# Optimization experiments

Hardware: AMD Instinct MI355X
Metric: run time of the kernel (lower is better)

The kernel has to match this reference:

```python
import jax, jax.numpy as jnp
import numpy as np

B, T, D = 2, 2048, 2048
N, K, H = 16, 4, 128  # query heads, kv heads, head dim
G = N // K            # GQA groups
MIN_TS, MAX_TS = 1.0, 10000.0


def rope(x, positions):
    # x: [B, S, heads, H], positions: [B, S] int
    half = H // 2
    fraction = 2.0 * jnp.arange(half, dtype=jnp.float32) / H
    timescale = MIN_TS * (MAX_TS / MIN_TS) ** fraction            # [half]
    sinusoid = positions.astype(jnp.float32)[:, :, None, None] / timescale  # [B,S,1,half]
    sin, cos = jnp.sin(sinusoid), jnp.cos(sinusoid)
    x1, x2 = x[..., :half], x[..., half:]
    return jnp.concatenate([x1 * cos - x2 * sin, x2 * cos + x1 * sin], axis=-1)


def setup_inputs() -> dict:
    key = jax.random.key(0)
    ks = jax.random.split(key, 6)
    pos = jnp.tile(jnp.arange(T, dtype=jnp.int32)[None, :], (B, 1))
    return {
        "Xq": jax.random.normal(ks[0], (B, T, D), jnp.float32),
        "Xkv": jax.random.normal(ks[1], (B, T, D), jnp.float32),
        "q_positions": pos,
        "kv_positions": pos,
        "Wq": jax.random.normal(ks[2], (D, N, H), jnp.float32) * 0.02,
        "Wk": jax.random.normal(ks[3], (D, K, H), jnp.float32) * 0.02,
        "Wv": jax.random.normal(ks[4], (D, K, H), jnp.float32) * 0.02,
        "Wo": jax.random.normal(ks[5], (N, H, D), jnp.float32) * 0.02,
    }


def reference(Xq, Xkv, q_positions, kv_positions, Wq, Wk, Wv, Wo):
    # QKV projections (tensordot over embed dim), fp32
    q = jnp.einsum("btd,dnh->btnh", Xq, Wq)          # [B,T,N,H]
    k = jnp.einsum("bsd,dkh->bskh", Xkv, Wk)         # [B,S,K,H]
    v = jnp.einsum("bsd,dkh->bskh", Xkv, Wv)
    # inline RoPE on q and k
    q = rope(q, q_positions)
    k = rope(k, kv_positions)
    # GQA: group query heads over kv heads -> [B,K,G,T,H]
    qg = q.transpose(0, 2, 1, 3).reshape(B, K, G, T, H)
    kt = k.transpose(0, 2, 1, 3)                      # [B,K,S,H]
    vt = v.transpose(0, 2, 1, 3)
    scale = 1.0 / jnp.sqrt(jnp.float32(H))
    scores = jnp.einsum("bkgth,bksh->bkgts", qg, kt) * scale
    # causal mask (self-attn, no explicit mask, T>1)
    causal = jnp.tril(jnp.ones((T, T), dtype=bool))
    scores = jnp.where(causal[None, None, None], scores, jnp.finfo(scores.dtype).min)
    probs = jax.nn.softmax(scores, axis=-1)
    attn = jnp.einsum("bkgts,bksh->bkgth", probs, vt)  # [B,K,G,T,H]
    attn = attn.reshape(B, N, T, H).transpose(0, 2, 1, 3)  # [B,T,N,H]
    out = jnp.einsum("btnh,nhd->btd", attn, Wo)
    return out
```

## Files before the change

### kernel.cpp

```cpp
#include <hip/hip_runtime.h>
#include <hip/hip_bf16.h>
#include <cstdint>
#include <cstddef>

#define Bdim 2
#define Tdim 2048
#define Ddim 2048
#define NHq  16
#define NKV  4
#define HD   128
#define SCALE 0.08838834764831845f
#define QPRESCALE (0.08838834764831845f * 1.4426950408889634f)
#define NEG_INF (-3.0e38f)
#define DEFER_THR 11.5f
#define ROPE_L2 0.20762051f
#define INV_2PI 0.15915494f

typedef unsigned short u16;
typedef unsigned int   u32;
typedef __bf16 bf16x8 __attribute__((ext_vector_type(8)));
typedef float  f32x4  __attribute__((ext_vector_type(4)));

__device__ __forceinline__ u16 f2bf(float f) {
    unsigned int u = __float_as_uint(f);
    u += 0x7FFFu + ((u >> 16) & 1u);
    return (u16)(u >> 16);
}
__device__ __forceinline__ u16 f2bfn(float f) {
    __bf16 h = (__bf16)f;
    return __builtin_bit_cast(u16, h);
}
__device__ __forceinline__ float bf2f(u16 s) {
    return __uint_as_float(((unsigned int)s) << 16);
}

__device__ __forceinline__ void hw_sincos_rev(float rev, float* s, float* c) {
    rev -= floorf(rev);
    *s = __builtin_amdgcn_sinf(rev);
    *c = __builtin_amdgcn_cosf(rev);
}

#if __has_builtin(__builtin_amdgcn_permlane16_swap) && __has_builtin(__builtin_amdgcn_permlane32_swap)
#define HAVE_PERMLANE_SWAP 1
#endif

__device__ __forceinline__ float quad_reduce_max(float v) {
#ifdef HAVE_PERMLANE_SWAP
    auto r = __builtin_amdgcn_permlane16_swap(__float_as_uint(v), __float_as_uint(v), false, false);
    float m = fmaxf(__uint_as_float(r[0]), __uint_as_float(r[1]));
    auto r2 = __builtin_amdgcn_permlane32_swap(__float_as_uint(m), __float_as_uint(m), false, false);
    return fmaxf(__uint_as_float(r2[0]), __uint_as_float(r2[1]));
#else
    v = fmaxf(v, __shfl_xor(v, 16));
    return fmaxf(v, __shfl_xor(v, 32));
#endif
}
__device__ __forceinline__ float quad_reduce_sum(float v) {
#ifdef HAVE_PERMLANE_SWAP
    auto r = __builtin_amdgcn_permlane16_swap(__float_as_uint(v), __float_as_uint(v), false, false);
    float s = __uint_as_float(r[0]) + __uint_as_float(r[1]);
    auto r2 = __builtin_amdgcn_permlane32_swap(__float_as_uint(s), __float_as_uint(s), false, false);
    return __uint_as_float(r2[0]) + __uint_as_float(r2[1]);
#else
    v += __shfl_xor(v, 16);
    return v + __shfl_xor(v, 32);
#endif
}

__device__ __forceinline__ float tree_max16(const float (&s)[16]) {
    float a0 = fmaxf(s[0], s[1]),  a1 = fmaxf(s[2], s[3]);
    float a2 = fmaxf(s[4], s[5]),  a3 = fmaxf(s[6], s[7]);
    float a4 = fmaxf(s[8], s[9]),  a5 = fmaxf(s[10], s[11]);
    float a6 = fmaxf(s[12], s[13]), a7 = fmaxf(s[14], s[15]);
    float b0 = fmaxf(a0, a1), b1 = fmaxf(a2, a3);
    float b2 = fmaxf(a4, a5), b3 = fmaxf(a6, a7);
    return fmaxf(fmaxf(b0, b1), fmaxf(b2, b3));
}
__device__ __forceinline__ float tree_sum16(const float (&s)[16]) {
    float a0 = s[0] + s[1],  a1 = s[2] + s[3];
    float a2 = s[4] + s[5],  a3 = s[6] + s[7];
    float a4 = s[8] + s[9],  a5 = s[10] + s[11];
    float a6 = s[12] + s[13], a7 = s[14] + s[15];
    float b0 = a0 + a1, b1 = a2 + a3, b2 = a4 + a5, b3 = a6 + a7;
    return (b0 + b1) + (b2 + b3);
}

typedef __attribute__((address_space(1))) const u32 gbl_u32;
typedef __attribute__((address_space(3))) u32 lds_u32;
__device__ __forceinline__ void gload16(const void* g, void* l) {
    __builtin_amdgcn_global_load_lds((gbl_u32*)(uintptr_t)g, (lds_u32*)(uintptr_t)l, 16, 0, 0);
}

#define VM8 asm volatile("s_waitcnt vmcnt(8)" ::: "memory")
#define VM6 asm volatile("s_waitcnt vmcnt(6)" ::: "memory")
#define VM4 asm volatile("s_waitcnt vmcnt(4)" ::: "memory")
#define VM3 asm volatile("s_waitcnt vmcnt(3)" ::: "memory")
#define VM0 asm volatile("s_waitcnt vmcnt(0)" ::: "memory")
#define VMNONE ((void)0)
#define BARRIER do { asm volatile("" ::: "memory"); __builtin_amdgcn_s_barrier(); asm volatile("" ::: "memory"); } while (0)

__global__ __launch_bounds__(256) void prep_all(const float* __restrict__ Xq,
                                                const float* __restrict__ Xkv,
                                                const float* __restrict__ Wq,
                                                const float* __restrict__ Wk,
                                                const float* __restrict__ Wv,
                                                const float* __restrict__ Wo,
                                                u16* __restrict__ xq_bf,
                                                u16* __restrict__ xkv_bf,
                                                u16* __restrict__ wq_t,
                                                u16* __restrict__ wk_t,
                                                u16* __restrict__ wv_t,
                                                u16* __restrict__ wo_t)
{
    __shared__ u16 t[64][72];
    const int tid = threadIdx.x;
    int bid = blockIdx.x;

    if (bid < 8192) {
        const size_t NE = (size_t)4096 * 2048 / 8;
        size_t idx = (size_t)bid * 256 + tid;
        const float* src; u16* dst; size_t off;
        if (idx < NE) { src = Xq;  dst = xq_bf;  off = idx * 8; }
        else          { src = Xkv; dst = xkv_bf; off = (idx - NE) * 8; }
        float4 a = *(const float4*)&src[off];
        float4 b = *(const float4*)&src[off + 4];
        ushort4 r0, r1;
        r0.x = f2bf(a.x); r0.y = f2bf(a.y); r0.z = f2bf(a.z); r0.w = f2bf(a.w);
        r1.x = f2bf(b.x); r1.y = f2bf(b.y); r1.z = f2bf(b.z); r1.w = f2bf(b.w);
        *(ushort4*)&dst[off] = r0;
        *(ushort4*)&dst[off + 4] = r1;
        return;
    }
    bid -= 8192;
    const float* src; u16* dst; int C, gx;
    const int R = 2048;
    if (bid < 1024)      { src = Wq; dst = wq_t; C = 2048; gx = 32; }
    else if (bid < 1280) { src = Wk; dst = wk_t; C = 512;  gx = 8;  bid -= 1024; }
    else if (bid < 1536) { src = Wv; dst = wv_t; C = 512;  gx = 8;  bid -= 1280; }
    else                 { src = Wo; dst = wo_t; C = 2048; gx = 32; bid -= 1536; }

    const int r0 = (bid / gx) * 64, c0 = (bid % gx) * 64;
    const int tr = tid >> 4, tc4 = (tid & 15) * 4;
#pragma unroll
    for (int p = 0; p < 4; p++) {
        int r = p * 16 + tr;
        float4 v = *(const float4*)&src[(size_t)(r0 + r) * C + c0 + tc4];
        t[tc4 + 0][r] = f2bf(v.x);
        t[tc4 + 1][r] = f2bf(v.y);
        t[tc4 + 2][r] = f2bf(v.z);
        t[tc4 + 3][r] = f2bf(v.w);
    }
    __syncthreads();
#pragma unroll
    for (int p = 0; p < 4; p++) {
        int cc = p * 16 + tr;
        ushort4 w = *(const ushort4*)&t[cc][tc4];
        *(ushort4*)&dst[(size_t)(c0 + cc) * R + r0 + tc4] = w;
    }
}

__global__ __launch_bounds__(256) void rope_k(u16* __restrict__ k,
                                              const int* __restrict__ kvpos)
{
    int idx = blockIdx.x * 256 + threadIdx.x;
    int rn = idx >> 4;
    int h4 = (idx & 15) * 4;
    int pos = kvpos[rn >> 2];
    u16* base = k + (size_t)rn * HD;
    ushort4 a = *(const ushort4*)&base[h4];
    ushort4 bvec = *(const ushort4*)&base[h4 + 64];
    u16 av[4] = {a.x, a.y, a.z, a.w};
    u16 bv[4] = {bvec.x, bvec.y, bvec.z, bvec.w};
#pragma unroll
    for (int j = 0; j < 4; j++) {
        float rscale = __builtin_amdgcn_exp2f((float)(h4 + j) * -ROPE_L2) * INV_2PI;
        float s, c;
        hw_sincos_rev((float)pos * rscale, &s, &c);
        float x1 = bf2f(av[j]), x2 = bf2f(bv[j]);
        av[j] = f2bf(x1 * c - x2 * s);
        bv[j] = f2bf(x2 * c + x1 * s);
    }
    ushort4 ra, rb;
    ra.x = av[0]; ra.y = av[1]; ra.z = av[2]; ra.w = av[3];
    rb.x = bv[0]; rb.y = bv[1]; rb.z = bv[2]; rb.w = bv[3];
    *(ushort4*)&base[h4] = ra;
    *(ushort4*)&base[h4 + 64] = rb;
}

#define GPH(c, ks, mh, STAGE, VMW) do {                                        \
    bf16x8 Af[4];                                                              \
    _Pragma("unroll")                                                          \
    for (int mf = 0; mf < 4; mf++)                                             \
        Af[mf] = *(const bf16x8*)&Ab[c][ks][(arow + (mh) * 64 + mf * 16) * 32 + cxs]; \
    if ((mh) == 0) {                                                           \
        _Pragma("unroll")                                                      \
        for (int nf = 0; nf < 4; nf++)                                         \
            Bf[nf] = *(const bf16x8*)&Bb[c][ks][(brow + nf * 16) * 32 + cxs];  \
    }                                                                          \
    STAGE;                                                                     \
    BARRIER;                                                                   \
    asm volatile("s_waitcnt lgkmcnt(0)" ::: "memory");                         \
    __builtin_amdgcn_s_setprio(1);                                             \
    _Pragma("unroll")                                                          \
    for (int mf = 0; mf < 4; mf++)                                             \
        _Pragma("unroll")                                                      \
        for (int nf = 0; nf < 4; nf++)                                         \
            acc[(mh) * 4 + mf][nf] = __builtin_amdgcn_mfma_f32_16x16x32_bf16(  \
                Af[mf], Bf[nf], acc[(mh) * 4 + mf][nf], 0, 0, 0);              \
    __builtin_amdgcn_s_setprio(0);                                             \
    VMW;                                                                       \
    BARRIER;                                                                   \
} while (0)

__device__ __forceinline__ void gemm8_mainloop(const u16* __restrict__ A,
                                               const u16* __restrict__ Bt,
                                               int m0, int n0,
                                               u16 (&Ab)[2][2][256 * 32],
                                               u16 (&Bb)[2][2][256 * 32],
                                               f32x4 (&acc)[8][4])
{
    const int tid = threadIdx.x;
    const int wv = tid >> 6, lane = tid & 63;
    const int l15 = lane & 15, quad = lane >> 4;
    const int wr = wv >> 2, wc = wv & 3;

#pragma unroll
    for (int mf = 0; mf < 8; mf++)
#pragma unroll
        for (int nf = 0; nf < 4; nf++) acc[mf][nf] = (f32x4){0.f, 0.f, 0.f, 0.f};

    auto stageA = [&](int kt, int kh, int c) {
#pragma unroll
        for (int j = 0; j < 2; j++) {
            int q = j * 512 + tid;
            int r = q >> 2;
            int c4 = (q & 3) ^ (r & 3);
            gload16(A + (size_t)(m0 + r) * 2048 + kt * 64 + kh * 32 + c4 * 8,
                    &Ab[c][kh][q * 8]);
        }
    };
    auto stageB = [&](int kt, int kh, int c) {
#pragma unroll
        for (int j = 0; j < 2; j++) {
            int q = j * 512 + tid;
            int r = q >> 2;
            int c4 = (q & 3) ^ (r & 3);
            gload16(Bt + (size_t)(n0 + r) * 2048 + kt * 64 + kh * 32 + c4 * 8,
                    &Bb[c][kh][q * 8]);
        }
    };

    const int arow = wr * 128 + l15;
    const int brow = wc * 64 + l15;
    const int cxs  = (quad ^ (l15 & 3)) * 8;

    stageA(0, 0, 0); stageB(0, 0, 0);
    stageA(0, 1, 0); stageB(0, 1, 0);
    stageA(1, 0, 1); stageB(1, 0, 1);
    VM8;
    BARRIER;

    bf16x8 Bf[4];
    for (int it = 0; it < 15; it++) {
        const int t0 = 2 * it, t1 = 2 * it + 1;
        GPH(0, 0, 0, { stageA(t1, 1, 1); },     VMNONE);
        GPH(0, 0, 1, { stageB(t1, 1, 1); },     VM8);
        GPH(0, 1, 0, { stageA(t0 + 2, 0, 0); }, VMNONE);
        GPH(0, 1, 1, { stageB(t0 + 2, 0, 0); }, VM8);
        GPH(1, 0, 0, { stageA(t0 + 2, 1, 0); }, VMNONE);
        GPH(1, 0, 1, { stageB(t0 + 2, 1, 0); }, VM8);
        GPH(1, 1, 0, { stageA(t1 + 2, 0, 1); }, VMNONE);
        GPH(1, 1, 1, { stageB(t1 + 2, 0, 1); }, VM8);
    }
    GPH(0, 0, 0, { stageA(31, 1, 1); }, VMNONE);
    GPH(0, 0, 1, { stageB(31, 1, 1); }, VM8);
    GPH(0, 1, 0, VMNONE, VMNONE);
    GPH(0, 1, 1, VMNONE, VM4);
    GPH(1, 0, 0, VMNONE, VMNONE);
    GPH(1, 0, 1, VMNONE, VM0);
    GPH(1, 1, 0, VMNONE, VMNONE);
    GPH(1, 1, 1, VMNONE, VMNONE);
}

__global__ __launch_bounds__(512, 2) void qkv_gemm8(const u16* __restrict__ Xq,
                                                    const u16* __restrict__ Xkv,
                                                    const u16* __restrict__ Wqt,
                                                    const u16* __restrict__ Wkt,
                                                    const u16* __restrict__ Wvt,
                                                    u16* __restrict__ qraw,
                                                    u16* __restrict__ kraw,
                                                    u16* __restrict__ vt)
{
    __shared__ __align__(16) u16 Ab[2][2][256 * 32];
    __shared__ __align__(16) u16 Bb[2][2][256 * 32];
    f32x4 acc[8][4];

    const int bid0 = (int)blockIdx.x + 12 * (int)blockIdx.y;
    const int swz  = (bid0 & 7) * 24 + (bid0 >> 3);
    const int cx   = swz % 12;
    const int m0   = (swz / 12) * 256;

    const u16 *A, *Bt; int nb;
    if (cx < 8)       { A = Xq;  Bt = Wqt; nb = cx * 256; }
    else if (cx < 10) { A = Xkv; Bt = Wkt; nb = (cx - 8) * 256; }
    else              { A = Xkv; Bt = Wvt; nb = (cx - 10) * 256; }

    gemm8_mainloop(A, Bt, m0, nb, Ab, Bb, acc);

    const int tid = threadIdx.x;
    const int wv = tid >> 6, lane = tid & 63;
    const int l15 = lane & 15, quad = lane >> 4;
    const int wr = wv >> 2, wc = wv & 3;
    const int row0 = m0 + wr * 128;

    if (cx < 10) {
        u16* out; int ldw;
        if (cx < 8) { out = qraw; ldw = 2048; }
        else        { out = kraw; ldw = 512; }
#pragma unroll
        for (int mf = 0; mf < 8; mf++)
#pragma unroll
            for (int nf = 0; nf < 4; nf++) {
                int col = nb + wc * 64 + nf * 16 + l15;
                int r = row0 + mf * 16 + quad * 4;
#pragma unroll
                for (int reg = 0; reg < 4; reg++)
                    out[(size_t)(r + reg) * ldw + col] = f2bf(acc[mf][nf][reg]);
            }
    } else {
        const int b = m0 >> 11;
#pragma unroll
        for (int mf = 0; mf < 8; mf++)
#pragma unroll
            for (int nf = 0; nf < 4; nf++) {
                int col = nb + wc * 64 + nf * 16 + l15;
                int tloc = ((row0 & 2047) + mf * 16 + quad * 4);
                ushort4 w4;
                w4.x = f2bf(acc[mf][nf][0]);
                w4.y = f2bf(acc[mf][nf][1]);
                w4.z = f2bf(acc[mf][nf][2]);
                w4.w = f2bf(acc[mf][nf][3]);
                *(ushort4*)&vt[((size_t)(b * 512 + col)) * 2048 + tloc] = w4;
            }
    }
}

#define GPHN(c, ks, mh, STAGE, VMW) do {                                       \
    bf16x8 Af[4];                                                              \
    _Pragma("unroll")                                                          \
    for (int mf = 0; mf < 4; mf++)                                             \
        Af[mf] = *(const bf16x8*)&Ab[c][ks][(arow + (mh) * 64 + mf * 16) * 32 + cxs]; \
    if ((mh) == 0) {                                                           \
        _Pragma("unroll")                                                      \
        for (int nf = 0; nf < 2; nf++)                                         \
            Bf[nf] = *(const bf16x8*)&Bb[c][ks][(brow + nf * 16) * 32 + cxs];  \
    }                                                                          \
    STAGE;                                                                     \
    BARRIER;                                                                   \
    asm volatile("s_waitcnt lgkmcnt(0)" ::: "memory");                         \
    __builtin_amdgcn_s_setprio(1);                                             \
    _Pragma("unroll")                                                          \
    for (int mf = 0; mf < 4; mf++)                                             \
        _Pragma("unroll")                                                      \
        for (int nf = 0; nf < 2; nf++)                                         \
            acc[(mh) * 4 + mf][nf] = __builtin_amdgcn_mfma_f32_16x16x32_bf16(  \
                Af[mf], Bf[nf], acc[(mh) * 4 + mf][nf], 0, 0, 0);              \
    __builtin_amdgcn_s_setprio(0);                                             \
    VMW;                                                                       \
    BARRIER;                                                                   \
} while (0)

__device__ __forceinline__ void gemm8n_mainloop(const u16* __restrict__ A,
                                                const u16* __restrict__ Bt,
                                                int m0, int n0,
                                                u16 (&Ab)[2][2][256 * 32],
                                                u16 (&Bb)[2][2][128 * 32],
                                                f32x4 (&acc)[8][2])
{
    const int tid = threadIdx.x;
    const int wv = tid >> 6, lane = tid & 63;
    const int l15 = lane & 15, quad = lane >> 4;
    const int wr = wv >> 2, wc = wv & 3;

#pragma unroll
    for (int mf = 0; mf < 8; mf++)
#pragma unroll
        for (int nf = 0; nf < 2; nf++) acc[mf][nf] = (f32x4){0.f, 0.f, 0.f, 0.f};

    auto stageA = [&](int kt, int kh, int c) {
#pragma unroll
        for (int j = 0; j < 2; j++) {
            int q = j * 512 + tid;
            int r = q >> 2;
            int c4 = (q & 3) ^ (r & 3);
            gload16(A + (size_t)(m0 + r) * 2048 + kt * 64 + kh * 32 + c4 * 8,
                    &Ab[c][kh][q * 8]);
        }
    };
    auto stageB = [&](int kt, int kh, int c) {
        int q = tid;
        int r = q >> 2;
        int c4 = (q & 3) ^ (r & 3);
        gload16(Bt + (size_t)(n0 + r) * 2048 + kt * 64 + kh * 32 + c4 * 8,
                &Bb[c][kh][q * 8]);
    };

    const int arow = wr * 128 + l15;
    const int brow = wc * 32 + l15;
    const int cxs  = (quad ^ (l15 & 3)) * 8;

    stageA(0, 0, 0); stageB(0, 0, 0);
    stageA(0, 1, 0); stageB(0, 1, 0);
    stageA(1, 0, 1); stageB(1, 0, 1);
    VM6;
    BARRIER;

    bf16x8 Bf[2];
    for (int it = 0; it < 15; it++) {
        const int t0 = 2 * it, t1 = 2 * it + 1;
        GPHN(0, 0, 0, { stageA(t1, 1, 1); },     VMNONE);
        GPHN(0, 0, 1, { stageB(t1, 1, 1); },     VM6);
        GPHN(0, 1, 0, { stageA(t0 + 2, 0, 0); }, VMNONE);
        GPHN(0, 1, 1, { stageB(t0 + 2, 0, 0); }, VM6);
        GPHN(1, 0, 0, { stageA(t0 + 2, 1, 0); }, VMNONE);
        GPHN(1, 0, 1, { stageB(t0 + 2, 1, 0); }, VM6);
        GPHN(1, 1, 0, { stageA(t1 + 2, 0, 1); }, VMNONE);
        GPHN(1, 1, 1, { stageB(t1 + 2, 0, 1); }, VM6);
    }
    GPHN(0, 0, 0, { stageA(31, 1, 1); }, VMNONE);
    GPHN(0, 0, 1, { stageB(31, 1, 1); }, VM6);
    GPHN(0, 1, 0, VMNONE, VMNONE);
    GPHN(0, 1, 1, VMNONE, VM3);
    GPHN(1, 0, 0, VMNONE, VMNONE);
    GPHN(1, 0, 1, VMNONE, VM0);
    GPHN(1, 1, 0, VMNONE, VMNONE);
    GPHN(1, 1, 1, VMNONE, VMNONE);
}

__global__ __launch_bounds__(512, 2) void oproj_gemm8n(const u16* __restrict__ attnb,
                                                       const u16* __restrict__ Wot,
                                                       float* __restrict__ out)
{
    __shared__ __align__(16) u16 Ab[2][2][256 * 32];
    __shared__ __align__(16) u16 Bb[2][2][128 * 32];
    f32x4 acc[8][2];

    const int bid0 = (int)blockIdx.x + 16 * (int)blockIdx.y;
    const int swz  = (bid0 & 7) * 32 + (bid0 >> 3);
    const int n0   = (swz % 16) * 128;
    const int m0   = (swz / 16) * 256;

    gemm8n_mainloop(attnb, Wot, m0, n0, Ab, Bb, acc);

    const int tid = threadIdx.x;
    const int wv = tid >> 6, lane = tid & 63;
    const int l15 = lane & 15, quad = lane >> 4;
    const int wr = wv >> 2, wc = wv & 3;
    const int row0 = m0 + wr * 128;
#pragma unroll
    for (int mf = 0; mf < 8; mf++)
#pragma unroll
        for (int nf = 0; nf < 2; nf++) {
            int col = n0 + wc * 32 + nf * 16 + l15;
            int r = row0 + mf * 16 + quad * 4;
#pragma unroll
            for (int reg = 0; reg < 4; reg++)
                out[(size_t)(r + reg) * 2048 + col] = acc[mf][nf][reg];
        }
}

__global__ __launch_bounds__(512, 4) void flash_attn_v7(const u16* __restrict__ qh,
                                                        const u16* __restrict__ kh,
                                                        const u16* __restrict__ vtg,
                                                        const int* __restrict__ qpos,
                                                        u16* __restrict__ attnb)
{
    __shared__ __align__(16) u16 Ks[2][64 * 128];
    __shared__ __align__(16) u16 Vt[2][128 * 64];
    __shared__ __align__(16) u16 Ps[128 * 64];

    const int yy = blockIdx.y;
    const int qt = (yy < 8) ? (15 - yy) : (yy - 8);
    const int bh = blockIdx.x;
    const int b = bh >> 4, n = bh & 15, kvh = n >> 2;
    const int q0 = qt * 128;
    const int tid = threadIdx.x;
    const int wv = tid >> 6, lane = tid & 63;
    const int l15 = lane & 15, quad = lane >> 4;

    const size_t kbase = (size_t)(b * Tdim) * 512 + kvh * 128;
    const size_t vbase = ((size_t)(b * 512 + kvh * 128)) * 2048;
    const int nT = 2 * qt + 2;

    auto stage = [&](int t, int buf) {
        const int s0s = t * 64;
#pragma unroll
        for (int c = 0; c < 2; c++) {
            int j = c * 512 + tid;
            int s = j >> 4;
            int c8 = (j & 15) ^ (s & 7);
            gload16(kh + kbase + (size_t)(s0s + s) * 512 + c8 * 8,
                    &Ks[buf][(c * 512 + wv * 64) * 8]);
            int h = j >> 3;
            int sb = (j & 7) ^ (h & 7);
            gload16(vtg + vbase + (size_t)h * 2048 + s0s + sb * 8,
                    &Vt[buf][(c * 512 + wv * 64) * 8]);
        }
    };

    stage(0, 0);

    bf16x8 qfrag[4];
    {
        const size_t qbase = ((size_t)(b * Tdim + q0 + wv * 16)) * 2048 + n * 128;
#pragma unroll
        for (int kt = 0; kt < 4; kt++)
            qfrag[kt] = *(const bf16x8*)(qh + qbase + (size_t)l15 * 2048
                                          + kt * 32 + quad * 8);
        const float fpos = (float)qpos[b * Tdim + q0 + wv * 16 + l15];
#pragma unroll
        for (int kt = 0; kt < 2; kt++)
#pragma unroll
            for (int j = 0; j < 8; j++) {
                int h = kt * 32 + quad * 8 + j;
                float rscale = __builtin_amdgcn_exp2f((float)h * -ROPE_L2) * INV_2PI;
                float s, c;
                hw_sincos_rev(fpos * rscale, &s, &c);
                s *= QPRESCALE; c *= QPRESCALE;
                float x1 = (float)qfrag[kt][j], x2 = (float)qfrag[kt + 2][j];
                qfrag[kt][j]     = (__bf16)(x1 * c - x2 * s);
                qfrag[kt + 2][j] = (__bf16)(x2 * c + x1 * s);
            }
    }

    f32x4 Oacc[8];
#pragma unroll
    for (int ht = 0; ht < 8; ht++) Oacc[ht] = (f32x4){0.f, 0.f, 0.f, 0.f};
    float mrow = NEG_INF;
    float lrow = 0.f;

    __syncthreads();

    int cur = 0;
    for (int t = 0; t < nT; t++) {
        const int s0 = t * 64;

        if (t + 1 < nT) stage(t + 1, cur ^ 1);

        f32x4 S[4];
#pragma unroll
        for (int nt = 0; nt < 4; nt++) S[nt] = (f32x4){0.f, 0.f, 0.f, 0.f};
#pragma unroll
        for (int kt = 0; kt < 4; kt++) {
            bf16x8 kf[4];
#pragma unroll
            for (int nt = 0; nt < 4; nt++) {
                int s = nt * 16 + l15;
                int cb = (kt * 4 + quad) ^ (s & 7);
                kf[nt] = *(const bf16x8*)&Ks[cur][s * 128 + cb * 8];
            }
#pragma unroll
            for (int nt = 0; nt < 4; nt++)
                S[nt] = __builtin_amdgcn_mfma_f32_16x16x32_bf16(kf[nt], qfrag[kt], S[nt], 0, 0, 0);
        }

        const bool domask = (t >= nT - 2);
        const int m_l = wv * 16 + l15;
        const int mg = q0 + m_l;
        float sv[16];
#pragma unroll
        for (int nt = 0; nt < 4; nt++)
#pragma unroll
            for (int r = 0; r < 4; r++) {
                float vv = S[nt][r];
                if (domask) {
                    int sg = s0 + nt * 16 + quad * 4 + r;
                    if (sg > mg) vv = NEG_INF;
                }
                sv[nt * 4 + r] = vv;
            }
        float mx = quad_reduce_max(tree_max16(sv));
        const bool skip = __all(mx <= mrow + DEFER_THR);
        const float mNew = skip ? mrow : fmaxf(mrow, mx);
#pragma unroll
        for (int i = 0; i < 16; i++)
            sv[i] = __builtin_amdgcn_exp2f(sv[i] - mNew);
#pragma unroll
        for (int nt = 0; nt < 4; nt++) {
            int sb = nt * 2 + (quad >> 1);
            int cb = sb ^ (m_l & 7);
            ushort4 pw;
            pw.x = f2bfn(sv[nt * 4 + 0]);
            pw.y = f2bfn(sv[nt * 4 + 1]);
            pw.z = f2bfn(sv[nt * 4 + 2]);
            pw.w = f2bfn(sv[nt * 4 + 3]);
            *(ushort4*)&Ps[m_l * 64 + cb * 8 + (quad & 1) * 4] = pw;
        }
        {
            float ps = quad_reduce_sum(tree_sum16(sv));
            if (skip) {
                lrow += ps;
            } else {
                float alpha = __builtin_amdgcn_exp2f(mrow - mNew);
                mrow = mNew;
                lrow = lrow * alpha + ps;
                float a0 = __shfl(alpha, quad * 4 + 0);
                float a1 = __shfl(alpha, quad * 4 + 1);
                float a2 = __shfl(alpha, quad * 4 + 2);
                float a3 = __shfl(alpha, quad * 4 + 3);
#pragma unroll
                for (int ht = 0; ht < 8; ht++) {
                    Oacc[ht][0] *= a0;
                    Oacc[ht][1] *= a1;
                    Oacc[ht][2] *= a2;
                    Oacc[ht][3] *= a3;
                }
            }
        }

#pragma unroll
        for (int k2 = 0; k2 < 2; k2++) {
            int cbp = (k2 * 4 + quad) ^ (m_l & 7);
            bf16x8 pf = *(const bf16x8*)&Ps[m_l * 64 + cbp * 8];
#pragma unroll
            for (int ht = 0; ht < 8; ht++) {
                int h = ht * 16 + l15;
                int cb = (k2 * 4 + quad) ^ (h & 7);
                bf16x8 vf = *(const bf16x8*)&Vt[cur][h * 64 + cb * 8];
                Oacc[ht] = __builtin_amdgcn_mfma_f32_16x16x32_bf16(pf, vf, Oacc[ht], 0, 0, 0);
            }
        }

        __syncthreads();
        cur ^= 1;
    }

    {
        f32x4 inv;
#pragma unroll
        for (int r = 0; r < 4; r++)
            inv[r] = 1.0f / __shfl(lrow, quad * 4 + r);
        int mg0 = q0 + wv * 16 + quad * 4;
        u16* dst0 = attnb + ((size_t)(b * Tdim + mg0)) * 2048 + n * 128 + l15;
#pragma unroll
        for (int ht = 0; ht < 8; ht++) {
#pragma unroll
            for (int r = 0; r < 4; r++)
                dst0[(size_t)r * 2048 + ht * 16] = f2bfn(Oacc[ht][r] * inv[r]);
        }
    }
}

extern "C" void kernel_launch(void* const* d_in, const int* in_sizes, int n_in,
                              void* d_out, int out_size, void* d_ws, size_t ws_size,
                              hipStream_t stream) {
    const float* Xq    = (const float*)d_in[0];
    const float* Xkv   = (const float*)d_in[1];
    const int*   qpos  = (const int*)d_in[2];
    const int*   kvpos = (const int*)d_in[3];
    const float* Wq    = (const float*)d_in[4];
    const float* Wk    = (const float*)d_in[5];
    const float* Wv    = (const float*)d_in[6];
    const float* Wo    = (const float*)d_in[7];
    float* out = (float*)d_out;

    char* w = (char*)d_ws;
    u16* xq_bf = (u16*)(w);
    u16* xkv_bf= (u16*)(w + (16u << 20));
    u16* qraw  = (u16*)(w + (32u << 20));
    u16* kraw  = (u16*)(w + (48u << 20));
    u16* vt    = (u16*)(w + (52u << 20));
    u16* wq_t  = (u16*)(w + (56u << 20));
    u16* wk_t  = (u16*)(w + (64u << 20));
    u16* wv_t  = (u16*)(w + (66u << 20));
    u16* wo_t  = (u16*)(w + (68u << 20));
    u16* attnb = (u16*)(w);

    prep_all<<<10752, 256, 0, stream>>>(Xq, Xkv, Wq, Wk, Wv, Wo,
                                        xq_bf, xkv_bf, wq_t, wk_t, wv_t, wo_t);
    qkv_gemm8<<<dim3(12, 16), 512, 0, stream>>>(xq_bf, xkv_bf, wq_t, wk_t, wv_t,
                                                qraw, kraw, vt);
    rope_k<<<1024, 256, 0, stream>>>(kraw, kvpos);
    flash_attn_v7<<<dim3(32, 16), 512, 0, stream>>>(qraw, kraw, vt, qpos, attnb);
    oproj_gemm8n<<<dim3(16, 16), 512, 0, stream>>>(attnb, wo_t, out);
}
```

Measured before the change: 308.8 us.

## Split K/V waits in flash attention and remap blocks by KV head

The attention kernel now issues the K and V tile prefetches separately. At the end of each iteration it waits only for the K tile. The wait for the V tile moves to just before the P·V matmul, so the V load can overlap the QK^T and softmax work. The grid is also flattened and remapped so that blocks sharing a batch and KV head run next to each other, which should improve L2 reuse of K/V. This adds an extra barrier per iteration and depends on hand-counted vmcnt values being correct.

```diff
diff --git a/kernel.cpp b/kernel.cpp
--- a/kernel.cpp
+++ b/kernel.cpp
@@ -95,6 +95,7 @@
 #define VM6 asm volatile("s_waitcnt vmcnt(6)" ::: "memory")
 #define VM4 asm volatile("s_waitcnt vmcnt(4)" ::: "memory")
 #define VM3 asm volatile("s_waitcnt vmcnt(3)" ::: "memory")
+#define VM2 asm volatile("s_waitcnt vmcnt(2)" ::: "memory")
 #define VM0 asm volatile("s_waitcnt vmcnt(0)" ::: "memory")
 #define VMNONE ((void)0)
 #define BARRIER do { asm volatile("" ::: "memory"); __builtin_amdgcn_s_barrier(); asm volatile("" ::: "memory"); } while (0)
@@ -469,7 +470,7 @@
         }
 }
 
-__global__ __launch_bounds__(512, 4) void flash_attn_v7(const u16* __restrict__ qh,
+__global__ __launch_bounds__(512, 4) void flash_attn_v8(const u16* __restrict__ qh,
                                                         const u16* __restrict__ kh,
                                                         const u16* __restrict__ vtg,
                                                         const int* __restrict__ qpos,
@@ -479,10 +480,13 @@
     __shared__ __align__(16) u16 Vt[2][128 * 64];
     __shared__ __align__(16) u16 Ps[128 * 64];
 
-    const int yy = blockIdx.y;
-    const int qt = (yy < 8) ? (15 - yy) : (yy - 8);
-    const int bh = blockIdx.x;
-    const int b = bh >> 4, n = bh & 15, kvh = n >> 2;
+    const int lin = (int)blockIdx.x;
+    const int g   = lin & 7;
+    const int m   = lin >> 3;
+    const int b   = g >> 2, kvh = g & 3;
+    const int n   = kvh * 4 + (m & 3);
+    const int yy  = m >> 2;
+    const int qt  = (yy < 8) ? (15 - yy) : (yy - 8);
     const int q0 = qt * 128;
     const int tid = threadIdx.x;
     const int wv = tid >> 6, lane = tid & 63;
@@ -492,7 +496,7 @@
     const size_t vbase = ((size_t)(b * 512 + kvh * 128)) * 2048;
     const int nT = 2 * qt + 2;
 
-    auto stage = [&](int t, int buf) {
+    auto stageK = [&](int t, int buf) {
         const int s0s = t * 64;
 #pragma unroll
         for (int c = 0; c < 2; c++) {
@@ -501,6 +505,13 @@
             int c8 = (j & 15) ^ (s & 7);
             gload16(kh + kbase + (size_t)(s0s + s) * 512 + c8 * 8,
                     &Ks[buf][(c * 512 + wv * 64) * 8]);
+        }
+    };
+    auto stageV = [&](int t, int buf) {
+        const int s0s = t * 64;
+#pragma unroll
+        for (int c = 0; c < 2; c++) {
+            int j = c * 512 + tid;
             int h = j >> 3;
             int sb = (j & 7) ^ (h & 7);
             gload16(vtg + vbase + (size_t)h * 2048 + s0s + sb * 8,
@@ -508,7 +519,8 @@
         }
     };
 
-    stage(0, 0);
+    stageK(0, 0);
+    stageV(0, 0);
 
     bf16x8 qfrag[4];
     {
@@ -539,13 +551,15 @@
     float mrow = NEG_INF;
     float lrow = 0.f;
 
-    __syncthreads();
+    VM2;
+    BARRIER;
 
     int cur = 0;
     for (int t = 0; t < nT; t++) {
         const int s0 = t * 64;
-
-        if (t + 1 < nT) stage(t + 1, cur ^ 1);
+        const bool more = (t + 1 < nT);
+
+        if (more) { stageK(t + 1, cur ^ 1); stageV(t + 1, cur ^ 1); }
 
         f32x4 S[4];
 #pragma unroll
@@ -618,6 +632,9 @@
             }
         }
 
+        if (more) { VM4; } else { VM0; }
+        BARRIER;
+
 #pragma unroll
         for (int k2 = 0; k2 < 2; k2++) {
             int cbp = (k2 * 4 + quad) ^ (m_l & 7);
@@ -631,7 +648,8 @@
             }
         }
 
-        __syncthreads();
+        if (more) { VM2; }
+        BARRIER;
         cur ^= 1;
     }
 
@@ -681,6 +699,6 @@
     qkv_gemm8<<<dim3(12, 16), 512, 0, stream>>>(xq_bf, xkv_bf, wq_t, wk_t, wv_t,
                                                 qraw, kraw, vt);
     rope_k<<<1024, 256, 0, stream>>>(kraw, kvpos);
-    flash_attn_v7<<<dim3(32, 16), 512, 0, stream>>>(qraw, kraw, vt, qpos, attnb);
+    flash_attn_v8<<<512, 512, 0, stream>>>(qraw, kraw, vt, qpos, attnb);
     oproj_gemm8n<<<dim3(16, 16), 512, 0, stream>>>(attnb, wo_t, out);
 }
```

Result: slower. 315.2 us (+2.1%).
